# Kernel tuning notes

Hardware: AMD Instinct MI355X
Metric: run time of the kernel (lower is better)

## Reference

```python
import jax, jax.numpy as jnp
import numpy as np

B, C, H, W = 64, 256, 56, 56
HEADS, DH, WS = 16, 16, 7  # C = HEADS*DH
EPS = 1e-6


def setup_inputs() -> dict:
    key = jax.random.key(0)
    k1, k2, k3 = jax.random.split(key, 3)
    return {
        "x": jax.random.normal(k1, (B, C, H, W), jnp.float32),
        "bn_gamma": jnp.ones((C,), jnp.float32),
        "bn_beta": jnp.zeros((C,), jnp.float32),
        "bn_mean": jnp.zeros((C,), jnp.float32),
        "bn_var": jnp.ones((C,), jnp.float32),
        "qk_w": jax.random.normal(k2, (2 * C, C), jnp.float32) * 0.02,
        "v_w": jax.random.normal(k3, (C, C), jnp.float32) * 0.02,
    }


def reference(x, bn_gamma, bn_beta, bn_mean, bn_var, qk_w, v_w):
    Bb, Cc, Hh, Ww = x.shape
    scale = DH ** -0.5
    # eval-mode BatchNorm2d (eps=1e-6)
    inv = bn_gamma / jnp.sqrt(bn_var + EPS)
    xn = (x - bn_mean[:, None, None]) * inv[:, None, None] + bn_beta[:, None, None]
    # window partition: einops '(h1 n1)' -> h1 (window coord) OUTER, n1 INNER
    # i.e. strided/grid windows; H divisible by WS so no padding (pad_r=pad_b=0)
    n1, n2 = Hh // WS, Ww // WS
    t = xn.reshape(Bb, Cc, WS, n1, WS, n2).transpose(0, 3, 5, 2, 4, 1)  # (B,n1,n2,ws,ws,C)
    tok = t.reshape(Bb * n1 * n2, WS * WS, Cc)  # per-window tokens
    # qk: 1x1 conv == matmul; channel layout (qk, heads, dim_head)
    qk = (tok @ qk_w.T).reshape(-1, WS * WS, 2, HEADS, DH)
    q = qk[:, :, 0].transpose(0, 2, 1, 3)  # (nb, heads, hw, dh)
    k = qk[:, :, 1].transpose(0, 2, 1, 3)
    attn = jax.nn.softmax(jnp.einsum('bhqd,bhkd->bhqk', q, k) * scale, axis=-1)
    # v: 1x1 conv + ReLU (attn_pre=False path)
    v = jax.nn.relu(tok @ v_w.T).reshape(-1, WS * WS, HEADS, DH).transpose(0, 2, 1, 3)
    o = jnp.einsum('bhqk,bhkd->bhqd', attn, v)  # (nb, heads, hw, dh)
    o = o.transpose(0, 2, 1, 3).reshape(Bb, n1, n2, WS, WS, Cc)
    # inverse window merge: target (B, C, ws_h, n1, ws_w, n2) -> (B, C, H, W)
    out = o.transpose(0, 5, 3, 1, 4, 2).reshape(Bb, Cc, Hh, Ww)
    return out
```

## Files before the change

kernel.cpp:

```cpp
#include <hip/hip_runtime.h>


typedef unsigned short u16;
typedef __attribute__((ext_vector_type(4))) float f32x4;
typedef __attribute__((ext_vector_type(8))) short short8;
typedef __attribute__((ext_vector_type(4))) short short4b;

__device__ __forceinline__ u16 f2bf(float f) {
  union { float f; unsigned int i; } v; v.f = f;
  unsigned int r = v.i + 0x7fffu + ((v.i >> 16) & 1u);
  return (u16)(r >> 16);
}

__global__ __launch_bounds__(256) void k0_wpack(
    const float* __restrict__ qkw, const float* __restrict__ vw,
    u16* __restrict__ wb)
{
  int idx = blockIdx.x * 256 + threadIdx.x;
  int n = idx >> 5, oct = idx & 31;
  int head = n / 48, sub = n - head * 48;
  const float* src;
  if (sub < 16)      src = qkw + (size_t)(head * 16 + sub) * 256;
  else if (sub < 32) src = qkw + (size_t)(256 + head * 16 + (sub - 16)) * 256;
  else               src = vw  + (size_t)(head * 16 + (sub - 32)) * 256;
  src += oct * 8;
  float4 a = *(const float4*)src;
  float4 c = *(const float4*)(src + 4);
  uint4 pk;
  pk.x = (unsigned)f2bf(a.x) | ((unsigned)f2bf(a.y) << 16);
  pk.y = (unsigned)f2bf(a.z) | ((unsigned)f2bf(a.w) << 16);
  pk.z = (unsigned)f2bf(c.x) | ((unsigned)f2bf(c.y) << 16);
  pk.w = (unsigned)f2bf(c.z) | ((unsigned)f2bf(c.w) << 16);
  *(uint4*)(wb + (size_t)n * 256 + oct * 8) = pk;
}

__global__ __launch_bounds__(256) void k1_bn_gather(
    const float* __restrict__ x, const float* __restrict__ g,
    const float* __restrict__ be, const float* __restrict__ mu,
    const float* __restrict__ va, u16* __restrict__ aws)
{
  __shared__ u16 lds[56 * 264];
  const int tid = threadIdx.x;
  const int bx = blockIdx.x;
  const int ws_h = bx % 7, win_h = (bx / 7) % 8, b = bx / 56;
  const int h = ws_h * 8 + win_h;

  for (int it = 0; it < 7; ++it) {
    int idx = it * 256 + tid;
    int c = idx / 7, oct = idx % 7;
    const float* src = x + (size_t)(b * 256 + c) * 3136 + h * 56 + oct * 8;
    float4 p0 = *(const float4*)src;
    float4 p1 = *(const float4*)(src + 4);
    float inv = g[c] * rsqrtf(va[c] + 1e-6f);
    float sh = be[c] - mu[c] * inv;
    float vals[8] = { p0.x, p0.y, p0.z, p0.w, p1.x, p1.y, p1.z, p1.w };
#pragma unroll
    for (int j = 0; j < 8; ++j)
      lds[(oct * 8 + j) * 264 + c] = f2bf(fmaf(vals[j], inv, sh));
  }
  __syncthreads();

  const size_t t0 = (size_t)(b * 64 + win_h * 8) * 49;
  for (int it = 0; it < 7; ++it) {
    int idx = it * 256 + tid;
    int tl = idx >> 5, coct = idx & 31;
    int win_w = tl / 7, ws_w = tl - win_w * 7;
    int w = ws_w * 8 + win_w;
    uint4 v = *(const uint4*)&lds[w * 264 + coct * 8];
    size_t tp = t0 + (size_t)win_w * 49 + ws_h * 7 + ws_w;
    *(uint4*)(aws + tp * 256 + coct * 8) = v;
  }
}

__global__ __launch_bounds__(256, 4) void k2_fused(
    const u16* __restrict__ aws, const u16* __restrict__ wb,
    float* __restrict__ out)
{
  __shared__ u16 smem[18432];
  u16* sA = smem;
  u16* sB = smem + 4608;
  const int tid = threadIdx.x;
  const int lane = tid & 63, wv = tid >> 6;
  const int l15 = lane & 15, quad = lane >> 4, kbase = quad * 4;

  const int bid = blockIdx.x;
  const int L = (bid & 7) * 2048 + (bid >> 3);
  const int ww = L & 7, nb = (L >> 3) & 3, whg = L >> 5;
  const int wh = whg & 7, b = whg >> 3;
  const int tloc = (whg << 3) | ww;
  const size_t arow0 = (size_t)tloc * 49 * 256;
  const int nb0 = nb * 192;

  f32x4 acc[4][3];
#pragma unroll
  for (int i = 0; i < 4; ++i)
#pragma unroll
    for (int j = 0; j < 3; ++j) acc[i][j] = (f32x4)(0.0f);

  for (int kb = 0; kb < 4; ++kb) {
    __syncthreads();
#pragma unroll
    for (int it = 0; it < 2; ++it) {
      int idx = it * 256 + tid;
      int r = idx >> 3, oct = idx & 7;
      int rs = r < 49 ? r : 48;
      uint4 v = *(const uint4*)(aws + arow0 + (size_t)rs * 256 + kb * 64 + oct * 8);
      *(uint4*)&sA[r * 72 + oct * 8] = v;
    }
#pragma unroll
    for (int it = 0; it < 6; ++it) {
      int idx = it * 256 + tid;
      int r = idx >> 3, oct = idx & 7;
      uint4 v = *(const uint4*)(wb + (size_t)(nb0 + r) * 256 + kb * 64 + oct * 8);
      *(uint4*)&sB[r * 72 + oct * 8] = v;
    }
    __syncthreads();
#pragma unroll
    for (int ks = 0; ks < 2; ++ks) {
      int col = ks * 32 + quad * 8;
      short8 bf[3];
#pragma unroll
      for (int nt = 0; nt < 3; ++nt)
        bf[nt] = *(const short8*)&sB[(wv * 48 + nt * 16 + l15) * 72 + col];
#pragma unroll
      for (int mt = 0; mt < 4; ++mt) {
        short8 af = *(const short8*)&sA[(mt * 16 + l15) * 72 + col];
#pragma unroll
        for (int nt = 0; nt < 3; ++nt)
          acc[mt][nt] = __builtin_amdgcn_mfma_f32_16x16x32_bf16(
              af, bf[nt], acc[mt][nt], 0, 0, 0);
      }
    }
  }
  __syncthreads();

  u16* Qh = smem + wv * 3392;
  u16* Kh = Qh + 1280;
  u16* Vh = Kh + 1280;
#pragma unroll
  for (int mt = 0; mt < 4; ++mt) {
#pragma unroll
    for (int r = 0; r < 4; ++r) {
      int tok = mt * 16 + kbase + r;
      Qh[tok * 20 + l15] = f2bf(acc[mt][0][r]);
      Kh[tok * 20 + l15] = f2bf(acc[mt][1][r]);
    }
    int tok0 = mt * 16 + kbase;
    if (mt < 3 || quad == 0) {
      short4b pv;
#pragma unroll
      for (int r = 0; r < 4; ++r) pv[r] = (short)f2bf(fmaxf(acc[mt][2][r], 0.0f));
      *(short4b*)&Vh[l15 * 52 + tok0] = pv;
    }
  }

  const float SM = 0.36067376022224085f;
  short4b ka[4], vf[4];
#pragma unroll
  for (int t = 0; t < 4; ++t) {
    ka[t] = *(const short4b*)&Kh[(t * 16 + l15) * 20 + kbase];
    vf[t] = *(const short4b*)&Vh[l15 * 52 + t * 16 + kbase];
  }
  f32x4 zz = (f32x4)(0.0f);
  const size_t obase0 = (size_t)(b * 256 + nb * 64 + wv * 16) * 3136;

#pragma unroll
  for (int qh = 0; qh < 2; ++qh) {
    short4b qb[2];
#pragma unroll
    for (int ntl = 0; ntl < 2; ++ntl)
      qb[ntl] = *(const short4b*)&Qh[((qh * 2 + ntl) * 16 + l15) * 20 + kbase];

    f32x4 s[4][2];
#pragma unroll
    for (int mt = 0; mt < 4; ++mt)
#pragma unroll
      for (int ntl = 0; ntl < 2; ++ntl)
        s[mt][ntl] = __builtin_amdgcn_mfma_f32_16x16x16bf16_1k(
            ka[mt], qb[ntl], zz, 0, 0, 0);

    float inv_sum[2];
    short4b pf[4][2];
#pragma unroll
    for (int ntl = 0; ntl < 2; ++ntl) {
      float m = -1e30f;
#pragma unroll
      for (int mt = 0; mt < 4; ++mt)
#pragma unroll
        for (int r = 0; r < 4; ++r) {
          int kt = mt * 16 + kbase + r;
          float v = (kt < 49) ? s[mt][ntl][r] : -1e30f;
          m = fmaxf(m, v);
        }
      m = fmaxf(m, __shfl_xor(m, 16, 64));
      m = fmaxf(m, __shfl_xor(m, 32, 64));
      float sum = 0.0f;
#pragma unroll
      for (int mt = 0; mt < 4; ++mt)
#pragma unroll
        for (int r = 0; r < 4; ++r) {
          int kt = mt * 16 + kbase + r;
          float p = (kt < 49) ? exp2f((s[mt][ntl][r] - m) * SM) : 0.0f;
          sum += p;
          pf[mt][ntl][r] = (short)f2bf(p);
        }
      sum += __shfl_xor(sum, 16, 64);
      sum += __shfl_xor(sum, 32, 64);
      inv_sum[ntl] = 1.0f / sum;
    }

    f32x4 o[2];
#pragma unroll
    for (int ntl = 0; ntl < 2; ++ntl) o[ntl] = zz;
#pragma unroll
    for (int kt = 0; kt < 4; ++kt)
#pragma unroll
      for (int ntl = 0; ntl < 2; ++ntl)
        o[ntl] = __builtin_amdgcn_mfma_f32_16x16x16bf16_1k(
            vf[kt], pf[kt][ntl], o[ntl], 0, 0, 0);

#pragma unroll
    for (int ntl = 0; ntl < 2; ++ntl) {
      int q = qh * 32 + ntl * 16 + l15;
      if (q < 49) {
        int tsh = q / 7, tsw = q - tsh * 7;
        size_t pbase = obase0 + (size_t)(tsh * 8 + wh) * 56 + tsw * 8 + ww;
#pragma unroll
        for (int r = 0; r < 4; ++r)
          out[pbase + (size_t)(kbase + r) * 3136] = o[ntl][r] * inv_sum[ntl];
      }
    }
  }
}

extern "C" void kernel_launch(void* const* d_in, const int* in_sizes, int n_in,
                              void* d_out, int out_size, void* d_ws, size_t ws_size,
                              hipStream_t stream) {
  const float* x   = (const float*)d_in[0];
  const float* g   = (const float*)d_in[1];
  const float* be  = (const float*)d_in[2];
  const float* mu  = (const float*)d_in[3];
  const float* va  = (const float*)d_in[4];
  const float* qkw = (const float*)d_in[5];
  const float* vw  = (const float*)d_in[6];
  float* outp = (float*)d_out;

  const size_t AWS_BYTES = (size_t)200704 * 256 * 2;
  u16* aws = (u16*)d_ws;
  u16* wb  = (u16*)((char*)d_ws + AWS_BYTES);

  k0_wpack<<<96, 256, 0, stream>>>(qkw, vw, wb);
  k1_bn_gather<<<64 * 8 * 7, 256, 0, stream>>>(x, g, be, mu, va, aws);
  k2_fused<<<64 * 64 * 4, 256, 0, stream>>>(aws, wb, outp);
}
```

Before: 564.2 us.

## Pre-swizzle activations and weights into MFMA fragment layout, chunk by batch

Packing kernels now write activations and weights directly in per-lane MFMA fragment order, so the fused kernel loads one contiguous 32 KB window tile into LDS once and reads weight fragments straight from global memory with no per-k-block LDS staging or repeated barriers. The BN/pack kernel reads whole channel planes coalesced and writes the windowed layout, and the host splits the batch into chunks that fit the workspace. Occupancy hint raised to 5 blocks; the padded activation layout doubles intermediate size relative to 49 rows, and weight fragments now come through cache instead of LDS.

```diff
diff --git a/kernel.cpp b/kernel.cpp
--- a/kernel.cpp
+++ b/kernel.cpp
@@ -14,16 +14,19 @@
 
 __global__ __launch_bounds__(256) void k0_wpack(
     const float* __restrict__ qkw, const float* __restrict__ vw,
-    u16* __restrict__ wb)
+    u16* __restrict__ w2)
 {
   int idx = blockIdx.x * 256 + threadIdx.x;
-  int n = idx >> 5, oct = idx & 31;
-  int head = n / 48, sub = n - head * 48;
+  int head = idx / 1536, r = idx - head * 1536;
+  int kb = r / 384;  r -= kb * 384;
+  int ks = r / 192;  r -= ks * 192;
+  int nt = r / 64;   int lq = r - nt * 64;
+  int l15 = lq >> 2, quad = lq & 3;
   const float* src;
-  if (sub < 16)      src = qkw + (size_t)(head * 16 + sub) * 256;
-  else if (sub < 32) src = qkw + (size_t)(256 + head * 16 + (sub - 16)) * 256;
-  else               src = vw  + (size_t)(head * 16 + (sub - 32)) * 256;
-  src += oct * 8;
+  if (nt == 0)      src = qkw + (size_t)(head * 16 + l15) * 256;
+  else if (nt == 1) src = qkw + (size_t)(256 + head * 16 + l15) * 256;
+  else              src = vw  + (size_t)(head * 16 + l15) * 256;
+  src += kb * 64 + ks * 32 + quad * 8;
   float4 a = *(const float4*)src;
   float4 c = *(const float4*)(src + 4);
   uint4 pk;
@@ -31,110 +34,124 @@
   pk.y = (unsigned)f2bf(a.z) | ((unsigned)f2bf(a.w) << 16);
   pk.z = (unsigned)f2bf(c.x) | ((unsigned)f2bf(c.y) << 16);
   pk.w = (unsigned)f2bf(c.z) | ((unsigned)f2bf(c.w) << 16);
-  *(uint4*)(wb + (size_t)n * 256 + oct * 8) = pk;
-}
-
-__global__ __launch_bounds__(256) void k1_bn_gather(
+  *(uint4*)(w2 + (size_t)idx * 8) = pk;
+}
+
+__global__ __launch_bounds__(256) void k1_bn_pack(
     const float* __restrict__ x, const float* __restrict__ g,
     const float* __restrict__ be, const float* __restrict__ mu,
-    const float* __restrict__ va, u16* __restrict__ aws)
+    const float* __restrict__ va, u16* __restrict__ a2, int b0)
 {
-  __shared__ u16 lds[56 * 264];
+  __shared__ u16 lds[8 * 3136];
+  __shared__ float sbn[16];
   const int tid = threadIdx.x;
-  const int bx = blockIdx.x;
-  const int ws_h = bx % 7, win_h = (bx / 7) % 8, b = bx / 56;
-  const int h = ws_h * 8 + win_h;
-
-  for (int it = 0; it < 7; ++it) {
-    int idx = it * 256 + tid;
-    int c = idx / 7, oct = idx % 7;
-    const float* src = x + (size_t)(b * 256 + c) * 3136 + h * 56 + oct * 8;
-    float4 p0 = *(const float4*)src;
-    float4 p1 = *(const float4*)(src + 4);
+  const int bid = blockIdx.x;
+  const int cpx = gridDim.x >> 3;
+  const int L = (bid & 7) * cpx + (bid >> 3);
+  const int coct = L & 31, bloc = L >> 5;
+  const int b = b0 + bloc;
+  const int c0 = coct * 8;
+
+  if (tid < 8) {
+    int c = c0 + tid;
     float inv = g[c] * rsqrtf(va[c] + 1e-6f);
-    float sh = be[c] - mu[c] * inv;
-    float vals[8] = { p0.x, p0.y, p0.z, p0.w, p1.x, p1.y, p1.z, p1.w };
-#pragma unroll
-    for (int j = 0; j < 8; ++j)
-      lds[(oct * 8 + j) * 264 + c] = f2bf(fmaf(vals[j], inv, sh));
-  }
-  __syncthreads();
-
-  const size_t t0 = (size_t)(b * 64 + win_h * 8) * 49;
-  for (int it = 0; it < 7; ++it) {
-    int idx = it * 256 + tid;
-    int tl = idx >> 5, coct = idx & 31;
-    int win_w = tl / 7, ws_w = tl - win_w * 7;
-    int w = ws_w * 8 + win_w;
-    uint4 v = *(const uint4*)&lds[w * 264 + coct * 8];
-    size_t tp = t0 + (size_t)win_w * 49 + ws_h * 7 + ws_w;
-    *(uint4*)(aws + tp * 256 + coct * 8) = v;
-  }
-}
-
-__global__ __launch_bounds__(256, 4) void k2_fused(
-    const u16* __restrict__ aws, const u16* __restrict__ wb,
-    float* __restrict__ out)
+    sbn[tid * 2] = inv;
+    sbn[tid * 2 + 1] = be[c] - mu[c] * inv;
+  }
+  __syncthreads();
+
+  const float* xp = x + (size_t)(b * 256 + c0) * 3136;
+  for (int i = tid; i < 6272; i += 256) {
+    int cl = i / 784, q = i - cl * 784;
+    float4 v = *(const float4*)(xp + (size_t)cl * 3136 + q * 4);
+    float inv = sbn[cl * 2], sh = sbn[cl * 2 + 1];
+    uint2 pk;
+    pk.x = (unsigned)f2bf(fmaf(v.x, inv, sh)) |
+           ((unsigned)f2bf(fmaf(v.y, inv, sh)) << 16);
+    pk.y = (unsigned)f2bf(fmaf(v.z, inv, sh)) |
+           ((unsigned)f2bf(fmaf(v.w, inv, sh)) << 16);
+    *(uint2*)&lds[cl * 3136 + q * 4] = pk;
+  }
+  __syncthreads();
+
+  const int kb = coct >> 3, ks = (coct >> 2) & 1, quad = coct & 3;
+  const int fo = (kb * 2 + ks) * 4;
+  u16* abase = a2 + (size_t)bloc * 64 * 16384;
+  for (int i = tid; i < 3136; i += 256) {
+    int win = i / 49, tok = i - win * 49;
+    int wh = win >> 3, ww = win & 7;
+    int wsh = tok / 7, wsw = tok - wsh * 7;
+    int px = (wsh * 8 + wh) * 56 + wsw * 8 + ww;
+    int mt = tok >> 4, l15 = tok & 15;
+    u16 e0 = lds[0 * 3136 + px], e1 = lds[1 * 3136 + px];
+    u16 e2 = lds[2 * 3136 + px], e3 = lds[3 * 3136 + px];
+    u16 e4 = lds[4 * 3136 + px], e5 = lds[5 * 3136 + px];
+    u16 e6 = lds[6 * 3136 + px], e7 = lds[7 * 3136 + px];
+    uint4 pk;
+    pk.x = (unsigned)e0 | ((unsigned)e1 << 16);
+    pk.y = (unsigned)e2 | ((unsigned)e3 << 16);
+    pk.z = (unsigned)e4 | ((unsigned)e5 << 16);
+    pk.w = (unsigned)e6 | ((unsigned)e7 << 16);
+    *(uint4*)(abase + (size_t)win * 16384 +
+              (fo + mt) * 512 + (l15 * 4 + quad) * 8) = pk;
+  }
+}
+
+__global__ __launch_bounds__(256, 5) void k2_fused(
+    const u16* __restrict__ a2, const u16* __restrict__ w2,
+    float* __restrict__ out, int b0)
 {
-  __shared__ u16 smem[18432];
-  u16* sA = smem;
-  u16* sB = smem + 4608;
+  __shared__ u16 smem[16448];
   const int tid = threadIdx.x;
   const int lane = tid & 63, wv = tid >> 6;
   const int l15 = lane & 15, quad = lane >> 4, kbase = quad * 4;
-
   const int bid = blockIdx.x;
-  const int L = (bid & 7) * 2048 + (bid >> 3);
+  const int cpx = gridDim.x >> 3;
+  const int L = (bid & 7) * cpx + (bid >> 3);
   const int ww = L & 7, nb = (L >> 3) & 3, whg = L >> 5;
-  const int wh = whg & 7, b = whg >> 3;
-  const int tloc = (whg << 3) | ww;
-  const size_t arow0 = (size_t)tloc * 49 * 256;
-  const int nb0 = nb * 192;
-
+  const int wh = whg & 7, bloc = whg >> 3;
+  const int b = b0 + bloc;
+  const int tloc = bloc * 64 + wh * 8 + ww;
+  const int head = nb * 4 + wv;
+
+  const u16* asrc = a2 + (size_t)tloc * 16384;
+#pragma unroll
+  for (int it = 0; it < 8; ++it) {
+    int chunk = it * 256 + tid;
+    *(uint4*)&smem[chunk * 8] = *(const uint4*)(asrc + chunk * 8);
+  }
+  __syncthreads();
+
+  const int laneoff = (l15 * 4 + quad) * 8;
+  const u16* wp = w2 + (size_t)head * 12288 + laneoff;
   f32x4 acc[4][3];
 #pragma unroll
   for (int i = 0; i < 4; ++i)
 #pragma unroll
     for (int j = 0; j < 3; ++j) acc[i][j] = (f32x4)(0.0f);
 
-  for (int kb = 0; kb < 4; ++kb) {
-    __syncthreads();
-#pragma unroll
-    for (int it = 0; it < 2; ++it) {
-      int idx = it * 256 + tid;
-      int r = idx >> 3, oct = idx & 7;
-      int rs = r < 49 ? r : 48;
-      uint4 v = *(const uint4*)(aws + arow0 + (size_t)rs * 256 + kb * 64 + oct * 8);
-      *(uint4*)&sA[r * 72 + oct * 8] = v;
-    }
-#pragma unroll
-    for (int it = 0; it < 6; ++it) {
-      int idx = it * 256 + tid;
-      int r = idx >> 3, oct = idx & 7;
-      uint4 v = *(const uint4*)(wb + (size_t)(nb0 + r) * 256 + kb * 64 + oct * 8);
-      *(uint4*)&sB[r * 72 + oct * 8] = v;
-    }
-    __syncthreads();
+#pragma unroll
+  for (int kb = 0; kb < 4; ++kb)
 #pragma unroll
     for (int ks = 0; ks < 2; ++ks) {
-      int col = ks * 32 + quad * 8;
-      short8 bf[3];
+      int fo = kb * 2 + ks;
+      short8 bf[3], af[4];
 #pragma unroll
       for (int nt = 0; nt < 3; ++nt)
-        bf[nt] = *(const short8*)&sB[(wv * 48 + nt * 16 + l15) * 72 + col];
-#pragma unroll
-      for (int mt = 0; mt < 4; ++mt) {
-        short8 af = *(const short8*)&sA[(mt * 16 + l15) * 72 + col];
+        bf[nt] = *(const short8*)(wp + (fo * 3 + nt) * 512);
+#pragma unroll
+      for (int mt = 0; mt < 4; ++mt)
+        af[mt] = *(const short8*)&smem[(fo * 4 + mt) * 512 + laneoff];
+#pragma unroll
+      for (int mt = 0; mt < 4; ++mt)
 #pragma unroll
         for (int nt = 0; nt < 3; ++nt)
           acc[mt][nt] = __builtin_amdgcn_mfma_f32_16x16x32_bf16(
-              af, bf[nt], acc[mt][nt], 0, 0, 0);
-      }
-    }
-  }
-  __syncthreads();
-
-  u16* Qh = smem + wv * 3392;
+              af[mt], bf[nt], acc[mt][nt], 0, 0, 0);
+    }
+  __syncthreads();
+
+  u16* Qh = smem + wv * 4096;
   u16* Kh = Qh + 1280;
   u16* Vh = Kh + 1280;
 #pragma unroll
@@ -146,11 +163,16 @@
       Kh[tok * 20 + l15] = f2bf(acc[mt][1][r]);
     }
     int tok0 = mt * 16 + kbase;
-    if (mt < 3 || quad == 0) {
+    if (mt < 3) {
       short4b pv;
 #pragma unroll
       for (int r = 0; r < 4; ++r) pv[r] = (short)f2bf(fmaxf(acc[mt][2][r], 0.0f));
       *(short4b*)&Vh[l15 * 52 + tok0] = pv;
+    } else if (quad == 0) {
+      short4b pv;
+      pv[0] = (short)f2bf(fmaxf(acc[mt][2][0], 0.0f));
+      pv[1] = 0; pv[2] = 0; pv[3] = 0;
+      *(short4b*)&Vh[l15 * 52 + tok0] = pv;
     }
   }
 
@@ -159,7 +181,12 @@
 #pragma unroll
   for (int t = 0; t < 4; ++t) {
     ka[t] = *(const short4b*)&Kh[(t * 16 + l15) * 20 + kbase];
-    vf[t] = *(const short4b*)&Vh[l15 * 52 + t * 16 + kbase];
+    if (t < 3)
+      vf[t] = *(const short4b*)&Vh[l15 * 52 + t * 16 + kbase];
+    else if (quad == 0)
+      vf[t] = *(const short4b*)&Vh[l15 * 52 + 48];
+    else
+      vf[t] = (short4b)0;
   }
   f32x4 zz = (f32x4)(0.0f);
   const size_t obase0 = (size_t)(b * 256 + nb * 64 + wv * 16) * 3136;
@@ -245,11 +272,20 @@
   const float* vw  = (const float*)d_in[6];
   float* outp = (float*)d_out;
 
-  const size_t AWS_BYTES = (size_t)200704 * 256 * 2;
-  u16* aws = (u16*)d_ws;
-  u16* wb  = (u16*)((char*)d_ws + AWS_BYTES);
-
-  k0_wpack<<<96, 256, 0, stream>>>(qkw, vw, wb);
-  k1_bn_gather<<<64 * 8 * 7, 256, 0, stream>>>(x, g, be, mu, va, aws);
-  k2_fused<<<64 * 64 * 4, 256, 0, stream>>>(aws, wb, outp);
-}
+  const size_t W2_BYTES = (size_t)768 * 256 * 2;
+  const size_t PER_IMG  = (size_t)64 * 16384 * 2;
+  u16* w2 = (u16*)d_ws;
+  u16* a2 = (u16*)((char*)d_ws + W2_BYTES);
+
+  size_t avail = ws_size > W2_BYTES ? ws_size - W2_BYTES : 0;
+  int bchunk = (int)(avail / PER_IMG);
+  if (bchunk > 64) bchunk = 64;
+  if (bchunk < 1)  bchunk = 1;
+
+  k0_wpack<<<96, 256, 0, stream>>>(qkw, vw, w2);
+  for (int c = 0; c < 64; c += bchunk) {
+    int nb = (64 - c < bchunk) ? (64 - c) : bchunk;
+    k1_bn_pack<<<nb * 32, 256, 0, stream>>>(x, g, be, mu, va, a2, c);
+    k2_fused<<<nb * 256, 256, 0, stream>>>(a2, w2, outp, c);
+  }
+}
```

Measured after the change: 650.6 us. 15.3% more time.

## Switch token workspace to channel-octet-major layout with per-plane BN gather

Applied to the files above, without the earlier changes.

The BN+gather kernel now processes one batch and eight channels per block, reading whole contiguous channel planes into LDS and writing an octet-major workspace (32 channel octets × all tokens × 8 bf16). The fused GEMM/attention kernel's A-tile load is remapped to this layout, so each octet fetch is 64 consecutive tokens × 16 bytes. The aim is fully coalesced input reads and larger contiguous runs for the strided window gather. The cost is a larger LDS footprint per block (about 50KB), which may lower occupancy of the gather kernel, and scattered 2-byte LDS reads in the transpose.

```diff
diff --git a/kernel.cpp b/kernel.cpp
--- a/kernel.cpp
+++ b/kernel.cpp
@@ -34,46 +34,61 @@
   *(uint4*)(wb + (size_t)n * 256 + oct * 8) = pk;
 }
 
-__global__ __launch_bounds__(256) void k1_bn_gather(
+__global__ __launch_bounds__(256) void k1_bn_oct(
     const float* __restrict__ x, const float* __restrict__ g,
     const float* __restrict__ be, const float* __restrict__ mu,
-    const float* __restrict__ va, u16* __restrict__ aws)
+    const float* __restrict__ va, u16* __restrict__ aws2)
 {
-  __shared__ u16 lds[56 * 264];
+  __shared__ u16 lds[8 * 3136];
+  __shared__ float sbn[16];
   const int tid = threadIdx.x;
-  const int bx = blockIdx.x;
-  const int ws_h = bx % 7, win_h = (bx / 7) % 8, b = bx / 56;
-  const int h = ws_h * 8 + win_h;
-
-  for (int it = 0; it < 7; ++it) {
-    int idx = it * 256 + tid;
-    int c = idx / 7, oct = idx % 7;
-    const float* src = x + (size_t)(b * 256 + c) * 3136 + h * 56 + oct * 8;
-    float4 p0 = *(const float4*)src;
-    float4 p1 = *(const float4*)(src + 4);
+  const int bid = blockIdx.x;
+  const int b = bid >> 5, coct = bid & 31;
+  const int c0 = coct * 8;
+
+  if (tid < 8) {
+    int c = c0 + tid;
     float inv = g[c] * rsqrtf(va[c] + 1e-6f);
-    float sh = be[c] - mu[c] * inv;
-    float vals[8] = { p0.x, p0.y, p0.z, p0.w, p1.x, p1.y, p1.z, p1.w };
-#pragma unroll
-    for (int j = 0; j < 8; ++j)
-      lds[(oct * 8 + j) * 264 + c] = f2bf(fmaf(vals[j], inv, sh));
+    sbn[tid * 2] = inv;
+    sbn[tid * 2 + 1] = be[c] - mu[c] * inv;
   }
   __syncthreads();
 
-  const size_t t0 = (size_t)(b * 64 + win_h * 8) * 49;
-  for (int it = 0; it < 7; ++it) {
-    int idx = it * 256 + tid;
-    int tl = idx >> 5, coct = idx & 31;
-    int win_w = tl / 7, ws_w = tl - win_w * 7;
-    int w = ws_w * 8 + win_w;
-    uint4 v = *(const uint4*)&lds[w * 264 + coct * 8];
-    size_t tp = t0 + (size_t)win_w * 49 + ws_h * 7 + ws_w;
-    *(uint4*)(aws + tp * 256 + coct * 8) = v;
+  const float* xp = x + (size_t)(b * 256 + c0) * 3136;
+  for (int i = tid; i < 6272; i += 256) {
+    int cl = i / 784, q = i - cl * 784;
+    float4 v = *(const float4*)(xp + (size_t)cl * 3136 + q * 4);
+    float inv = sbn[cl * 2], sh = sbn[cl * 2 + 1];
+    uint2 pk;
+    pk.x = (unsigned)f2bf(fmaf(v.x, inv, sh)) |
+           ((unsigned)f2bf(fmaf(v.y, inv, sh)) << 16);
+    pk.y = (unsigned)f2bf(fmaf(v.z, inv, sh)) |
+           ((unsigned)f2bf(fmaf(v.w, inv, sh)) << 16);
+    *(uint2*)&lds[cl * 3136 + q * 4] = pk;
+  }
+  __syncthreads();
+
+  u16* abase = aws2 + ((size_t)coct * 200704 + (size_t)b * 3136) * 8;
+  for (int i = tid; i < 3136; i += 256) {
+    int win = i / 49, tok = i - win * 49;
+    int wh = win >> 3, ww = win & 7;
+    int wsh = tok / 7, wsw = tok - wsh * 7;
+    int px = (wsh * 8 + wh) * 56 + wsw * 8 + ww;
+    u16 e0 = lds[0 * 3136 + px], e1 = lds[1 * 3136 + px];
+    u16 e2 = lds[2 * 3136 + px], e3 = lds[3 * 3136 + px];
+    u16 e4 = lds[4 * 3136 + px], e5 = lds[5 * 3136 + px];
+    u16 e6 = lds[6 * 3136 + px], e7 = lds[7 * 3136 + px];
+    uint4 pk;
+    pk.x = (unsigned)e0 | ((unsigned)e1 << 16);
+    pk.y = (unsigned)e2 | ((unsigned)e3 << 16);
+    pk.z = (unsigned)e4 | ((unsigned)e5 << 16);
+    pk.w = (unsigned)e6 | ((unsigned)e7 << 16);
+    *(uint4*)(abase + (size_t)i * 8) = pk;
   }
 }
 
 __global__ __launch_bounds__(256, 4) void k2_fused(
-    const u16* __restrict__ aws, const u16* __restrict__ wb,
+    const u16* __restrict__ aws2, const u16* __restrict__ wb,
     float* __restrict__ out)
 {
   __shared__ u16 smem[18432];
@@ -88,7 +103,7 @@
   const int ww = L & 7, nb = (L >> 3) & 3, whg = L >> 5;
   const int wh = whg & 7, b = whg >> 3;
   const int tloc = (whg << 3) | ww;
-  const size_t arow0 = (size_t)tloc * 49 * 256;
+  const int t0 = tloc * 49;
   const int nb0 = nb * 192;
 
   f32x4 acc[4][3];
@@ -102,9 +117,10 @@
 #pragma unroll
     for (int it = 0; it < 2; ++it) {
       int idx = it * 256 + tid;
-      int r = idx >> 3, oct = idx & 7;
+      int oct = idx >> 6, r = idx & 63;
       int rs = r < 49 ? r : 48;
-      uint4 v = *(const uint4*)(aws + arow0 + (size_t)rs * 256 + kb * 64 + oct * 8);
+      uint4 v = *(const uint4*)(aws2 +
+          ((size_t)(kb * 8 + oct) * 200704 + t0 + rs) * 8);
       *(uint4*)&sA[r * 72 + oct * 8] = v;
     }
 #pragma unroll
@@ -245,11 +261,11 @@
   const float* vw  = (const float*)d_in[6];
   float* outp = (float*)d_out;
 
-  const size_t AWS_BYTES = (size_t)200704 * 256 * 2;
-  u16* aws = (u16*)d_ws;
-  u16* wb  = (u16*)((char*)d_ws + AWS_BYTES);
+  const size_t AWS2_BYTES = (size_t)32 * 200704 * 8 * 2;
+  u16* aws2 = (u16*)d_ws;
+  u16* wb   = (u16*)((char*)d_ws + AWS2_BYTES);
 
   k0_wpack<<<96, 256, 0, stream>>>(qkw, vw, wb);
-  k1_bn_gather<<<64 * 8 * 7, 256, 0, stream>>>(x, g, be, mu, va, aws);
-  k2_fused<<<64 * 64 * 4, 256, 0, stream>>>(aws, wb, outp);
-}
+  k1_bn_oct<<<64 * 32, 256, 0, stream>>>(x, g, be, mu, va, aws2);
+  k2_fused<<<64 * 64 * 4, 256, 0, stream>>>(aws2, wb, outp);
+}
```

New measurement: 568.1 us. No clear change (+0.7%).
